# Performance work log

Measured on AMD Instinct MI355X. Metric: run time of the kernel, lower is better.

Reference implementation:

```python
import jax, jax.numpy as jnp
import numpy as np

B = 4096          # batch
IN = 4096         # in_features
OUT = 4096        # out_features
MASK_DENSITY = 0.1

def setup_inputs() -> dict:
    key = jax.random.key(0)
    k1, k2, k3, k4, k5 = jax.random.split(key, 5)
    x = jax.random.normal(k1, (B, IN), dtype=jnp.float32)
    # truncated-normal-ish init, std 0.1 (plain normal scaled is fine for a numeric baseline)
    weight = jax.random.normal(k2, (OUT, IN), dtype=jnp.float32) * 0.1
    bound = 1.0 / np.sqrt(IN)
    bias = jax.random.uniform(k3, (OUT,), dtype=jnp.float32, minval=-bound, maxval=bound)
    mask = jax.random.bernoulli(k4, MASK_DENSITY, (OUT, IN))  # bool, fixed sparsity pattern
    residual_connection = jax.random.randint(k5, (OUT,), 0, IN, dtype=jnp.int32)
    return {"x": x, "weight": weight, "bias": bias, "mask": mask,
            "residual_connection": residual_connection}

def reference(x, weight, bias, mask, residual_connection):
    # out = relu(x @ (mask * W)^T + b) + x[:, residual_connection]
    w_masked = jnp.where(mask, weight, 0.0)              # [OUT, IN]
    out = x @ w_masked.T + bias                          # [B, OUT]
    out = jax.nn.relu(out)
    out = jnp.take(x, residual_connection, axis=1) + out # gathered residual add
    return out
```

## Files before the change

kernel.cpp:

```cpp
#include <hip/hip_runtime.h>
#include <hip/hip_bf16.h>
#include <stdint.h>

#define B_ROWS 4096
#define IN_F   4096
#define OUT_F  4096

#define BM 128
#define BN 128
#define BK 32

typedef float  f32x4  __attribute__((ext_vector_type(4)));
typedef short  bf16x8 __attribute__((ext_vector_type(8)));
typedef unsigned short u16x4 __attribute__((ext_vector_type(4)));

#define AS1 __attribute__((address_space(1)))
#define AS3 __attribute__((address_space(3)))

__device__ __forceinline__ uint16_t f2bf_rne(float f) {
    uint32_t u = __float_as_uint(f);
    uint32_t r = u + 0x7fffu + ((u >> 16) & 1u);
    return (uint16_t)(r >> 16);
}
__device__ __forceinline__ float bf2f(uint16_t h) {
    return __uint_as_float(((uint32_t)h) << 16);
}

__global__ __launch_bounds__(256) void cvt_x_t_kernel(
    const float* __restrict__ x, uint16_t* __restrict__ xb, uint16_t* __restrict__ xbT)
{
    __shared__ float t[64][65];
    const int r0 = blockIdx.y * 64;
    const int c0 = blockIdx.x * 64;
    const int tid = threadIdx.x;
    const int lr = tid >> 4;
    const int lc4 = (tid & 15) * 4;

#pragma unroll
    for (int p = 0; p < 4; ++p) {
        const int row = p * 16 + lr;
        float4 v = *(const float4*)(x + (size_t)(r0 + row) * IN_F + c0 + lc4);
        ushort4 o;
        o.x = f2bf_rne(v.x); o.y = f2bf_rne(v.y);
        o.z = f2bf_rne(v.z); o.w = f2bf_rne(v.w);
        *(ushort4*)(xb + (size_t)(r0 + row) * IN_F + c0 + lc4) = o;
        t[row][lc4 + 0] = v.x; t[row][lc4 + 1] = v.y;
        t[row][lc4 + 2] = v.z; t[row][lc4 + 3] = v.w;
    }
    __syncthreads();
#pragma unroll
    for (int p = 0; p < 4; ++p) {
        const int c = p * 16 + lr;
        ushort4 o;
        o.x = f2bf_rne(t[lc4 + 0][c]);
        o.y = f2bf_rne(t[lc4 + 1][c]);
        o.z = f2bf_rne(t[lc4 + 2][c]);
        o.w = f2bf_rne(t[lc4 + 3][c]);
        *(ushort4*)(xbT + (size_t)(c0 + c) * B_ROWS + r0 + lc4) = o;
    }
}

__global__ void detect_mask_kernel(const uint32_t* __restrict__ mraw, int* __restrict__ flag) {
    __shared__ uint32_t red[256];
    uint32_t acc = 0;
    for (int k = threadIdx.x; k < 1024; k += 256) acc |= mraw[k];
    red[threadIdx.x] = acc;
    __syncthreads();
    for (int s = 128; s > 0; s >>= 1) {
        if (threadIdx.x < s) red[threadIdx.x] |= red[threadIdx.x + s];
        __syncthreads();
    }
    if (threadIdx.x == 0) *flag = (red[0] & 0xFFFFFF00u) ? 1 : 0;
}

__global__ void cvt_w_kernel(const float* __restrict__ w, const void* __restrict__ mraw,
                             const int* __restrict__ flag, uint16_t* __restrict__ wb) {
    int i = (blockIdx.x * 256 + threadIdx.x) * 4;
    float4 v = *(const float4*)(w + i);
    int m0, m1, m2, m3;
    if (*flag) {
        uchar4 mm = *(const uchar4*)((const uint8_t*)mraw + i);
        m0 = mm.x; m1 = mm.y; m2 = mm.z; m3 = mm.w;
    } else {
        int4 mm = *(const int4*)((const int*)mraw + i);
        m0 = mm.x; m1 = mm.y; m2 = mm.z; m3 = mm.w;
    }
    ushort4 o;
    o.x = m0 ? f2bf_rne(v.x) : (uint16_t)0;
    o.y = m1 ? f2bf_rne(v.y) : (uint16_t)0;
    o.z = m2 ? f2bf_rne(v.z) : (uint16_t)0;
    o.w = m3 ? f2bf_rne(v.w) : (uint16_t)0;
    *(ushort4*)(wb + i) = o;
}

__global__ __launch_bounds__(256) void gemm_kernel(
    const uint16_t* __restrict__ xb, const uint16_t* __restrict__ wb,
    const uint16_t* __restrict__ xbT, const float* __restrict__ bias,
    const int* __restrict__ rc, float* __restrict__ out)
{
    __shared__ alignas(16) uint16_t As[BM * BK];
    __shared__ alignas(16) uint16_t Bs[BN * BK];
    __shared__ float bias_s[BN];
    __shared__ int   rc_s[BN];

    const int tid  = threadIdx.x;
    const int row0 = blockIdx.y * BM;
    const int col0 = blockIdx.x * BN;

    if (tid < BN) { bias_s[tid] = bias[col0 + tid]; rc_s[tid] = rc[col0 + tid]; }

    const int wave = tid >> 6, lane = tid & 63;
    const int wm = wave >> 1, wn = wave & 1;
    const int quad = lane >> 4, l16 = lane & 15;

    f32x4 acc[4][4];
#pragma unroll
    for (int i = 0; i < 4; ++i)
#pragma unroll
        for (int j = 0; j < 4; ++j)
            acc[i][j] = (f32x4){0.f, 0.f, 0.f, 0.f};

    for (int k0 = 0; k0 < IN_F; k0 += BK) {
#pragma unroll
        for (int it = 0; it < 2; ++it) {
            int c  = tid + it * 256;
            int r  = c >> 2;
            int kc = (c & 3) * 8;
            __builtin_amdgcn_global_load_lds(
                (const AS1 void*)(xb + (size_t)(row0 + r) * IN_F + k0 + kc),
                (AS3 void*)(As + c * 8), 16, 0, 0);
            __builtin_amdgcn_global_load_lds(
                (const AS1 void*)(wb + (size_t)(col0 + r) * IN_F + k0 + kc),
                (AS3 void*)(Bs + c * 8), 16, 0, 0);
        }
        __syncthreads();

        bf16x8 af[4], bfr[4];
#pragma unroll
        for (int i = 0; i < 4; ++i)
            af[i] = *(const bf16x8*)(As + (wm * 64 + i * 16 + l16) * BK + quad * 8);
#pragma unroll
        for (int j = 0; j < 4; ++j)
            bfr[j] = *(const bf16x8*)(Bs + (wn * 64 + j * 16 + l16) * BK + quad * 8);

#pragma unroll
        for (int i = 0; i < 4; ++i)
#pragma unroll
            for (int j = 0; j < 4; ++j)
                acc[i][j] = __builtin_amdgcn_mfma_f32_16x16x32_bf16(af[i], bfr[j], acc[i][j], 0, 0, 0);
        __syncthreads();
    }

#pragma unroll
    for (int j = 0; j < 4; ++j) {
        const int lcol = wn * 64 + j * 16 + l16;
        const int gcol = col0 + lcol;
        const float bv = bias_s[lcol];
        const int   rv = rc_s[lcol];
#pragma unroll
        for (int i = 0; i < 4; ++i) {
            const int grow0 = row0 + wm * 64 + i * 16 + quad * 4;
            u16x4 xq = *(const u16x4*)(xbT + (size_t)rv * B_ROWS + grow0);
#pragma unroll
            for (int r = 0; r < 4; ++r) {
                float v = fmaxf(acc[i][j][r] + bv, 0.0f) + bf2f(xq[r]);
                out[(size_t)(grow0 + r) * OUT_F + gcol] = v;
            }
        }
    }
}

extern "C" void kernel_launch(void* const* d_in, const int* in_sizes, int n_in,
                              void* d_out, int out_size, void* d_ws, size_t ws_size,
                              hipStream_t stream) {
    const float* x    = (const float*)d_in[0];
    const float* w    = (const float*)d_in[1];
    const float* bias = (const float*)d_in[2];
    const void*  mask = (const void*)d_in[3];
    const int*   rc   = (const int*)d_in[4];
    float* out = (float*)d_out;

    uint16_t* xb   = (uint16_t*)d_ws;
    uint16_t* wb   = xb  + (size_t)B_ROWS * IN_F;
    uint16_t* xbT  = wb  + (size_t)OUT_F * IN_F;
    int*      flag = (int*)(xbT + (size_t)IN_F * B_ROWS);

    detect_mask_kernel<<<1, 256, 0, stream>>>((const uint32_t*)mask, flag);
    {
        dim3 g(IN_F / 64, B_ROWS / 64);
        cvt_x_t_kernel<<<g, 256, 0, stream>>>(x, xb, xbT);
    }
    cvt_w_kernel<<<(OUT_F * IN_F) / (256 * 4), 256, 0, stream>>>(w, mask, flag, wb);

    dim3 grid(OUT_F / BN, B_ROWS / BM);
    gemm_kernel<<<grid, 256, 0, stream>>>(xb, wb, xbT, bias, rc, out);
}
```

Before: 412.8 us.

## Fuse prep kernels into one launch and swizzle GEMM tile order

Merges mask detection, x conversion/transpose and weight masking into a single prep kernel. Each weight block now detects the mask format locally, which removes the serial single-block detect launch and two extra kernel launches. The GEMM block index is remapped into an 8-way grouped swizzle so that concurrently running blocks share A and B tiles in L2/MALL. Every weight block now re-checks the format over its own chunk, and that check relies on a heuristic over only part of the mask.

```diff
diff --git a/kernel.cpp b/kernel.cpp
--- a/kernel.cpp
+++ b/kernel.cpp
@@ -26,71 +26,76 @@
     return __uint_as_float(((uint32_t)h) << 16);
 }
 
-__global__ __launch_bounds__(256) void cvt_x_t_kernel(
-    const float* __restrict__ x, uint16_t* __restrict__ xb, uint16_t* __restrict__ xbT)
+__global__ __launch_bounds__(256) void prep_kernel(
+    const float* __restrict__ x, const float* __restrict__ w,
+    const void* __restrict__ mraw,
+    uint16_t* __restrict__ xb, uint16_t* __restrict__ xbT,
+    uint16_t* __restrict__ wb)
 {
     __shared__ float t[64][65];
-    const int r0 = blockIdx.y * 64;
-    const int c0 = blockIdx.x * 64;
+    __shared__ int   sflag;
     const int tid = threadIdx.x;
-    const int lr = tid >> 4;
-    const int lc4 = (tid & 15) * 4;
-
-#pragma unroll
-    for (int p = 0; p < 4; ++p) {
-        const int row = p * 16 + lr;
-        float4 v = *(const float4*)(x + (size_t)(r0 + row) * IN_F + c0 + lc4);
-        ushort4 o;
-        o.x = f2bf_rne(v.x); o.y = f2bf_rne(v.y);
-        o.z = f2bf_rne(v.z); o.w = f2bf_rne(v.w);
-        *(ushort4*)(xb + (size_t)(r0 + row) * IN_F + c0 + lc4) = o;
-        t[row][lc4 + 0] = v.x; t[row][lc4 + 1] = v.y;
-        t[row][lc4 + 2] = v.z; t[row][lc4 + 3] = v.w;
+    const int bid = blockIdx.x;
+
+    if (bid < 4096) {
+        const int r0 = (bid >> 6) * 64;
+        const int c0 = (bid & 63) * 64;
+        const int lr  = tid >> 4;
+        const int lc4 = (tid & 15) * 4;
+#pragma unroll
+        for (int p = 0; p < 4; ++p) {
+            const int row = p * 16 + lr;
+            float4 v = *(const float4*)(x + (size_t)(r0 + row) * IN_F + c0 + lc4);
+            ushort4 o;
+            o.x = f2bf_rne(v.x); o.y = f2bf_rne(v.y);
+            o.z = f2bf_rne(v.z); o.w = f2bf_rne(v.w);
+            *(ushort4*)(xb + (size_t)(r0 + row) * IN_F + c0 + lc4) = o;
+            t[row][lc4 + 0] = v.x; t[row][lc4 + 1] = v.y;
+            t[row][lc4 + 2] = v.z; t[row][lc4 + 3] = v.w;
+        }
+        __syncthreads();
+#pragma unroll
+        for (int p = 0; p < 4; ++p) {
+            const int c = p * 16 + lr;
+            ushort4 o;
+            o.x = f2bf_rne(t[lc4 + 0][c]);
+            o.y = f2bf_rne(t[lc4 + 1][c]);
+            o.z = f2bf_rne(t[lc4 + 2][c]);
+            o.w = f2bf_rne(t[lc4 + 3][c]);
+            *(ushort4*)(xbT + (size_t)(c0 + c) * B_ROWS + r0 + lc4) = o;
+        }
+    } else {
+        const int e0 = (bid - 4096) * 4096;
+        if (tid == 0) sflag = 0;
+        __syncthreads();
+        {
+            const uint32_t* mw = (const uint32_t*)mraw + (e0 >> 2) + tid * 4;
+            uint4 sw = *(const uint4*)mw;
+            if ((sw.x | sw.y | sw.z | sw.w) & 0xFFFFFF00u) sflag = 1;
+        }
+        __syncthreads();
+        const int isbyte = sflag;
+        const int base = e0 + tid * 16;
+#pragma unroll
+        for (int q = 0; q < 4; ++q) {
+            const int i = base + q * 4;
+            float4 v = *(const float4*)(w + i);
+            int m0, m1, m2, m3;
+            if (isbyte) {
+                uchar4 mm = *(const uchar4*)((const uint8_t*)mraw + i);
+                m0 = mm.x; m1 = mm.y; m2 = mm.z; m3 = mm.w;
+            } else {
+                int4 mm = *(const int4*)((const int*)mraw + i);
+                m0 = mm.x; m1 = mm.y; m2 = mm.z; m3 = mm.w;
+            }
+            ushort4 o;
+            o.x = m0 ? f2bf_rne(v.x) : (uint16_t)0;
+            o.y = m1 ? f2bf_rne(v.y) : (uint16_t)0;
+            o.z = m2 ? f2bf_rne(v.z) : (uint16_t)0;
+            o.w = m3 ? f2bf_rne(v.w) : (uint16_t)0;
+            *(ushort4*)(wb + i) = o;
+        }
     }
-    __syncthreads();
-#pragma unroll
-    for (int p = 0; p < 4; ++p) {
-        const int c = p * 16 + lr;
-        ushort4 o;
-        o.x = f2bf_rne(t[lc4 + 0][c]);
-        o.y = f2bf_rne(t[lc4 + 1][c]);
-        o.z = f2bf_rne(t[lc4 + 2][c]);
-        o.w = f2bf_rne(t[lc4 + 3][c]);
-        *(ushort4*)(xbT + (size_t)(c0 + c) * B_ROWS + r0 + lc4) = o;
-    }
-}
-
-__global__ void detect_mask_kernel(const uint32_t* __restrict__ mraw, int* __restrict__ flag) {
-    __shared__ uint32_t red[256];
-    uint32_t acc = 0;
-    for (int k = threadIdx.x; k < 1024; k += 256) acc |= mraw[k];
-    red[threadIdx.x] = acc;
-    __syncthreads();
-    for (int s = 128; s > 0; s >>= 1) {
-        if (threadIdx.x < s) red[threadIdx.x] |= red[threadIdx.x + s];
-        __syncthreads();
-    }
-    if (threadIdx.x == 0) *flag = (red[0] & 0xFFFFFF00u) ? 1 : 0;
-}
-
-__global__ void cvt_w_kernel(const float* __restrict__ w, const void* __restrict__ mraw,
-                             const int* __restrict__ flag, uint16_t* __restrict__ wb) {
-    int i = (blockIdx.x * 256 + threadIdx.x) * 4;
-    float4 v = *(const float4*)(w + i);
-    int m0, m1, m2, m3;
-    if (*flag) {
-        uchar4 mm = *(const uchar4*)((const uint8_t*)mraw + i);
-        m0 = mm.x; m1 = mm.y; m2 = mm.z; m3 = mm.w;
-    } else {
-        int4 mm = *(const int4*)((const int*)mraw + i);
-        m0 = mm.x; m1 = mm.y; m2 = mm.z; m3 = mm.w;
-    }
-    ushort4 o;
-    o.x = m0 ? f2bf_rne(v.x) : (uint16_t)0;
-    o.y = m1 ? f2bf_rne(v.y) : (uint16_t)0;
-    o.z = m2 ? f2bf_rne(v.z) : (uint16_t)0;
-    o.w = m3 ? f2bf_rne(v.w) : (uint16_t)0;
-    *(ushort4*)(wb + i) = o;
 }
 
 __global__ __launch_bounds__(256) void gemm_kernel(
@@ -103,9 +108,14 @@
     __shared__ float bias_s[BN];
     __shared__ int   rc_s[BN];
 
-    const int tid  = threadIdx.x;
-    const int row0 = blockIdx.y * BM;
-    const int col0 = blockIdx.x * BN;
+    const int tid = threadIdx.x;
+    const int bid = blockIdx.y * gridDim.x + blockIdx.x;
+    const int r  = bid & 7;
+    const int s  = bid >> 3;
+    const int mt = (r >> 2) * 16 + (s & 15);
+    const int nt = (r & 3) * 8 + (s >> 4);
+    const int row0 = mt * BM;
+    const int col0 = nt * BN;
 
     if (tid < BN) { bias_s[tid] = bias[col0 + tid]; rc_s[tid] = rc[col0 + tid]; }
 
@@ -124,13 +134,13 @@
 #pragma unroll
         for (int it = 0; it < 2; ++it) {
             int c  = tid + it * 256;
-            int r  = c >> 2;
+            int rr = c >> 2;
             int kc = (c & 3) * 8;
             __builtin_amdgcn_global_load_lds(
-                (const AS1 void*)(xb + (size_t)(row0 + r) * IN_F + k0 + kc),
+                (const AS1 void*)(xb + (size_t)(row0 + rr) * IN_F + k0 + kc),
                 (AS3 void*)(As + c * 8), 16, 0, 0);
             __builtin_amdgcn_global_load_lds(
-                (const AS1 void*)(wb + (size_t)(col0 + r) * IN_F + k0 + kc),
+                (const AS1 void*)(wb + (size_t)(col0 + rr) * IN_F + k0 + kc),
                 (AS3 void*)(Bs + c * 8), 16, 0, 0);
         }
         __syncthreads();
@@ -162,9 +172,9 @@
             const int grow0 = row0 + wm * 64 + i * 16 + quad * 4;
             u16x4 xq = *(const u16x4*)(xbT + (size_t)rv * B_ROWS + grow0);
 #pragma unroll
-            for (int r = 0; r < 4; ++r) {
-                float v = fmaxf(acc[i][j][r] + bv, 0.0f) + bf2f(xq[r]);
-                out[(size_t)(grow0 + r) * OUT_F + gcol] = v;
+            for (int rr = 0; rr < 4; ++rr) {
+                float v = fmaxf(acc[i][j][rr] + bv, 0.0f) + bf2f(xq[rr]);
+                out[(size_t)(grow0 + rr) * OUT_F + gcol] = v;
             }
         }
     }
@@ -180,17 +190,11 @@
     const int*   rc   = (const int*)d_in[4];
     float* out = (float*)d_out;
 
-    uint16_t* xb   = (uint16_t*)d_ws;
-    uint16_t* wb   = xb  + (size_t)B_ROWS * IN_F;
-    uint16_t* xbT  = wb  + (size_t)OUT_F * IN_F;
-    int*      flag = (int*)(xbT + (size_t)IN_F * B_ROWS);
-
-    detect_mask_kernel<<<1, 256, 0, stream>>>((const uint32_t*)mask, flag);
-    {
-        dim3 g(IN_F / 64, B_ROWS / 64);
-        cvt_x_t_kernel<<<g, 256, 0, stream>>>(x, xb, xbT);
-    }
-    cvt_w_kernel<<<(OUT_F * IN_F) / (256 * 4), 256, 0, stream>>>(w, mask, flag, wb);
+    uint16_t* xb  = (uint16_t*)d_ws;
+    uint16_t* wb  = xb  + (size_t)B_ROWS * IN_F;
+    uint16_t* xbT = wb  + (size_t)OUT_F * IN_F;
+
+    prep_kernel<<<8192, 256, 0, stream>>>(x, w, mask, xb, xbT, wb);
 
     dim3 grid(OUT_F / BN, B_ROWS / BM);
     gemm_kernel<<<grid, 256, 0, stream>>>(xb, wb, xbT, bias, rc, out);
```

After: 422.0 us. +2.2%, slower.
